# Kernel tuning notes

Hardware: AMD Instinct MI355X
Metric: run time of the kernel (lower is better)

Reference implementation:

```python
import jax, jax.numpy as jnp
import numpy as np

B, D, K, H, E, Z = 64, 25000, 16, 128, 256, 32


def setup_inputs() -> dict:
    key = jax.random.key(0)
    ks = jax.random.split(key, 10)
    s = 0.02
    return {
        "x": jax.random.normal(ks[0], (B, D), jnp.float32),
        "mask": jax.random.randint(ks[1], (B, D), 0, 2, jnp.int32),
        "feat_emb": jax.random.normal(ks[2], (D, K), jnp.float32),          # feature_embedding [D,K]
        "feat_bias": jnp.zeros((D, 1), jnp.float32),                        # feature_bias [D,1]
        "W1": jax.random.normal(ks[3], (1 + K + 1, H), jnp.float32) * s,    # h_layer linear 1 (in,out)
        "b1": jnp.zeros((H,), jnp.float32),
        "W2": jax.random.normal(ks[4], (H, K), jnp.float32) * s,            # h_layer linear 2
        "b2": jnp.zeros((K,), jnp.float32),
        "We1": jax.random.normal(ks[5], (K, E), jnp.float32) * s,           # encoder_mlp linear 1
        "be1": jnp.zeros((E,), jnp.float32),
        "We2": jax.random.normal(ks[6], (E, 2 * Z), jnp.float32) * s,       # encoder_mlp linear 2
        "be2": jnp.zeros((2 * Z,), jnp.float32),
    }


def reference(x, mask, feat_emb, feat_bias, W1, b1, W2, b2, We1, be1, We2, be2):
    b, d = x.shape
    k = feat_emb.shape[1]
    # Build per-(sample, feature) input rows: [x_bd, F_d(K), bias_d] -> [B, D, 1+K+1]
    h_in = jnp.concatenate(
        [
            x[:, :, None],
            jnp.broadcast_to(feat_emb[None, :, :], (b, d, k)),
            jnp.broadcast_to(feat_bias[None, :, :], (b, d, 1)),
        ],
        axis=-1,
    )
    # Shared small MLP (h_layer), dropout is identity at rate 0.0
    h = jax.nn.relu(h_in @ W1 + b1)          # [B, D, H]
    h = jax.nn.relu(h @ W2 + b2)             # [B, D, K]
    # Masked sum pooling over features
    c = jnp.sum(h * mask.astype(h.dtype)[:, :, None], axis=1)  # [B, K]
    # encoder_mlp
    enc = jax.nn.relu(c @ We1 + be1) @ We2 + be2                # [B, 2Z]
    mu, logvar = jnp.split(enc, 2, axis=-1)
    return mu, logvar
```

## Files before the change

kernel.cpp:

```cpp
#include <hip/hip_runtime.h>

#define B 64
#define D 25000
#define K 16
#define H 128
#define E 256
#define Z 32
#define DTILE 16
#define NT_TILES ((D + DTILE - 1) / DTILE)
#define NPB 512
#define XSTR 68
#define MSTR 68

typedef __attribute__((ext_vector_type(8))) _Float16 half8;
typedef __attribute__((ext_vector_type(2))) _Float16 hv2;
typedef __attribute__((ext_vector_type(4))) float f32x4;

__global__ __launch_bounds__(256, 2) void main_kernel(
    const float* __restrict__ x, const int* __restrict__ mask,
    const float* __restrict__ feat_emb, const float* __restrict__ feat_bias,
    const float* __restrict__ W1, const float* __restrict__ b1,
    const float* __restrict__ W2, const float* __restrict__ b2,
    float* __restrict__ part)
{
    __shared__ __align__(16) _Float16 sGh[2][DTILE * H];
    __shared__ __align__(16) _Float16 sXh[2][DTILE * XSTR];
    __shared__ __align__(16) float    sMf[2][DTILE * MSTR];

    const int t    = threadIdx.x;
    const int lane = t & 63;
    const int wv   = t >> 6;
    const int g    = lane >> 4;
    const int n    = lane & 15;

    half8 Bf[4];
    #pragma unroll
    for (int s = 0; s < 4; ++s) {
        union { half8 v; _Float16 e[8]; } u;
        #pragma unroll
        for (int j = 0; j < 8; ++j)
            u.e[j] = (_Float16)W2[(s * 32 + g * 8 + j) * K + n];
        Bf[s] = u.v;
    }
    hv2 w0h[4][4];
    #pragma unroll
    for (int s = 0; s < 4; ++s) {
        const float4* wp = (const float4*)&W1[s * 32 + g * 8];
        float4 a0 = wp[0], a1 = wp[1];
        w0h[s][0] = (hv2){(_Float16)a0.x, (_Float16)a0.y};
        w0h[s][1] = (hv2){(_Float16)a0.z, (_Float16)a0.w};
        w0h[s][2] = (hv2){(_Float16)a1.x, (_Float16)a1.y};
        w0h[s][3] = (hv2){(_Float16)a1.z, (_Float16)a1.w};
    }
    half8 bfG[2];
    #pragma unroll
    for (int cc = 0; cc < 2; ++cc) {
        const int h = (wv * 2 + cc) * 16 + n;
        union { half8 v; _Float16 e[8]; } u;
        #pragma unroll
        for (int j = 0; j < 8; ++j) {
            const int k = g * 8 + j;
            float v;
            if (k < 16)       v = W1[(1 + k) * H + h];
            else if (k == 16) v = W1[17 * H + h];
            else if (k == 17) v = b1[h];
            else              v = 0.f;
            u.e[j] = (_Float16)v;
        }
        bfG[cc] = u.v;
    }
    const float b2n = b2[n];
    const hv2 zeroh = {(_Float16)0.f, (_Float16)0.f};
    const int moff = wv * 16 + g * 4;
    const int sample = wv * 16 + n;

    auto STAGE = [&](int buf, int tile) {
        const int bb = t >> 2;
        const int dd = (t & 3) * 4;
        const int dg = tile * DTILE + dd;
        float xv[4], mv[4];
        if (dg + 4 <= D) {
            float4 xx = *(const float4*)&x[(size_t)bb * D + dg];
            int4   mm = *(const int4*)&mask[(size_t)bb * D + dg];
            xv[0] = xx.x; xv[1] = xx.y; xv[2] = xx.z; xv[3] = xx.w;
            mv[0] = (float)mm.x; mv[1] = (float)mm.y; mv[2] = (float)mm.z; mv[3] = (float)mm.w;
        } else {
            #pragma unroll
            for (int i = 0; i < 4; ++i) {
                const int dgi = dg + i;
                xv[i] = (dgi < D) ? x[(size_t)bb * D + dgi] : 0.f;
                mv[i] = (dgi < D) ? (float)mask[(size_t)bb * D + dgi] : 0.f;
            }
        }
        #pragma unroll
        for (int i = 0; i < 4; ++i) {
            sXh[buf][(dd + i) * XSTR + bb] = (_Float16)xv[i];
            sMf[buf][(dd + i) * MSTR + bb] = mv[i];
        }
    };

    auto GCOMP = [&](int buf, int tile) {
        const int dA = min(tile * DTILE + n, D - 1);
        union { half8 v; _Float16 e[8]; } af;
        if (g < 2) {
            const float4* fe = (const float4*)&feat_emb[(size_t)dA * K + g * 8];
            float4 u0 = fe[0], u1 = fe[1];
            af.e[0] = (_Float16)u0.x; af.e[1] = (_Float16)u0.y;
            af.e[2] = (_Float16)u0.z; af.e[3] = (_Float16)u0.w;
            af.e[4] = (_Float16)u1.x; af.e[5] = (_Float16)u1.y;
            af.e[6] = (_Float16)u1.z; af.e[7] = (_Float16)u1.w;
        } else if (g == 2) {
            af.e[0] = (_Float16)feat_bias[dA];
            af.e[1] = (_Float16)1.f;
            #pragma unroll
            for (int j = 2; j < 8; ++j) af.e[j] = (_Float16)0.f;
        } else {
            #pragma unroll
            for (int j = 0; j < 8; ++j) af.e[j] = (_Float16)0.f;
        }
        #pragma unroll
        for (int cc = 0; cc < 2; ++cc) {
            f32x4 C = {0.f, 0.f, 0.f, 0.f};
            C = __builtin_amdgcn_mfma_f32_16x16x32_f16(af.v, bfG[cc], C, 0, 0, 0);
            #pragma unroll
            for (int r = 0; r < 4; ++r)
                sGh[buf][(g * 4 + r) * H + (wv * 2 + cc) * 16 + n] = (_Float16)C[r];
        }
    };

    f32x4 cacc = {0.f, 0.f, 0.f, 0.f};

    int tt = blockIdx.x;
    STAGE(0, tt);
    GCOMP(0, tt);
    __syncthreads();

    int cur = 0;
    for (; tt < NT_TILES; tt += NPB) {
        const int nxt = tt + NPB;
        if (nxt < NT_TILES) { STAGE(cur ^ 1, nxt); GCOMP(cur ^ 1, nxt); }

        hv2 xh[DTILE / 2];
        #pragma unroll
        for (int i = 0; i < DTILE / 2; ++i)
            xh[i] = (hv2){sXh[cur][(2 * i) * XSTR + sample],
                          sXh[cur][(2 * i + 1) * XSTR + sample]};
        const _Float16* gb0 = sGh[cur] + g * 8;

        #pragma unroll
        for (int i = 0; i < DTILE / 2; ++i) {
            const int dd0 = 2 * i, dd1 = 2 * i + 1;
            const hv2 xa = {xh[i].x, xh[i].x};
            const hv2 xb = {xh[i].y, xh[i].y};
            f32x4 c1a = {b2n, b2n, b2n, b2n};
            f32x4 c1b = {b2n, b2n, b2n, b2n};
            #pragma unroll
            for (int s = 0; s < 4; ++s) {
                union GA { half8 v; hv2 p[4]; };
                GA ga, gb, A0, A1;
                ga.v = *(const half8*)(gb0 + dd0 * H + s * 32);
                gb.v = *(const half8*)(gb0 + dd1 * H + s * 32);
                #pragma unroll
                for (int p = 0; p < 4; ++p) {
                    hv2 h0 = __builtin_elementwise_fma(xa, w0h[s][p], ga.p[p]);
                    hv2 h1 = __builtin_elementwise_fma(xb, w0h[s][p], gb.p[p]);
                    A0.p[p] = __builtin_elementwise_max(h0, zeroh);
                    A1.p[p] = __builtin_elementwise_max(h1, zeroh);
                }
                c1a = __builtin_amdgcn_mfma_f32_16x16x32_f16(A0.v, Bf[s], c1a, 0, 0, 0);
                c1b = __builtin_amdgcn_mfma_f32_16x16x32_f16(A1.v, Bf[s], c1b, 0, 0, 0);
            }
            float4 m0 = *(const float4*)&sMf[cur][dd0 * MSTR + moff];
            float4 m1 = *(const float4*)&sMf[cur][dd1 * MSTR + moff];
            cacc[0] = fmaf(m0.x, fmaxf(c1a[0], 0.f), fmaf(m1.x, fmaxf(c1b[0], 0.f), cacc[0]));
            cacc[1] = fmaf(m0.y, fmaxf(c1a[1], 0.f), fmaf(m1.y, fmaxf(c1b[1], 0.f), cacc[1]));
            cacc[2] = fmaf(m0.z, fmaxf(c1a[2], 0.f), fmaf(m1.z, fmaxf(c1b[2], 0.f), cacc[2]));
            cacc[3] = fmaf(m0.w, fmaxf(c1a[3], 0.f), fmaf(m1.w, fmaxf(c1b[3], 0.f), cacc[3]));
        }
        __syncthreads();
        cur ^= 1;
    }

    float* crep = part + (size_t)blockIdx.x * (B * K);
    #pragma unroll
    for (int r = 0; r < 4; ++r)
        crep[(moff + r) * K + n] = cacc[r];
}

__global__ __launch_bounds__(256) void partial_enc_kernel(
    const float* __restrict__ part, const float* __restrict__ We1,
    const float* __restrict__ be1, const float* __restrict__ We2,
    const float* __restrict__ be2, float* __restrict__ out)
{
    const int b = blockIdx.x;
    const int t = threadIdx.x;
    __shared__ float sc[K];
    __shared__ float st1[E];
    __shared__ float red[256];

    {
        const int k = t & 15;
        float acc0 = 0.f;
        #pragma unroll 4
        for (int p = t >> 4; p < NPB; p += 16)
            acc0 += part[(size_t)p * (B * K) + b * K + k];
        red[t] = acc0;
    }
    __syncthreads();
    if (t < K) {
        float s2 = 0.f;
        #pragma unroll
        for (int q = 0; q < 16; ++q) s2 += red[q * 16 + t];
        sc[t] = s2;
    }
    __syncthreads();

    {
        float acc = be1[t];
        #pragma unroll
        for (int k = 0; k < K; ++k)
            acc = fmaf(sc[k], We1[k * E + t], acc);
        st1[t] = fmaxf(acc, 0.f);
    }
    __syncthreads();

    const int j = t & 63, seg = t >> 6;
    float acc = 0.f;
    #pragma unroll 4
    for (int e = seg * 64; e < seg * 64 + 64; ++e)
        acc = fmaf(st1[e], We2[e * 64 + j], acc);
    red[t] = acc;
    __syncthreads();

    if (t < 64) {
        float v = red[j] + red[64 + j] + red[128 + j] + red[192 + j] + be2[j];
        if (j < Z) out[b * Z + j] = v;
        else       out[B * Z + b * Z + (j - Z)] = v;
    }
}

extern "C" void kernel_launch(void* const* d_in, const int* in_sizes, int n_in,
                              void* d_out, int out_size, void* d_ws, size_t ws_size,
                              hipStream_t stream) {
    const float* x         = (const float*)d_in[0];
    const int*   mask      = (const int*)  d_in[1];
    const float* feat_emb  = (const float*)d_in[2];
    const float* feat_bias = (const float*)d_in[3];
    const float* W1        = (const float*)d_in[4];
    const float* b1        = (const float*)d_in[5];
    const float* W2        = (const float*)d_in[6];
    const float* b2        = (const float*)d_in[7];
    const float* We1       = (const float*)d_in[8];
    const float* be1       = (const float*)d_in[9];
    const float* We2       = (const float*)d_in[10];
    const float* be2       = (const float*)d_in[11];

    float* part = (float*)d_ws;

    main_kernel<<<NPB, 256, 0, stream>>>(
        x, mask, feat_emb, feat_bias, W1, b1, W2, b2, part);
    partial_enc_kernel<<<B, 256, 0, stream>>>(
        part, We1, be1, We2, be2, (float*)d_out);
}
```

Measured before the change: 112.1 us.

## Split tile features across waves instead of samples and reduce partials in LDS

Each wave now handles 4 of the 16 features in a tile for all 64 samples, instead of 16 samples across all features. This lets each wave load the per-feature G vectors once and reuse them across four sample groups, and x is stored sample-major so it can be read as packed half4. Because waves now hold partial sums for the same outputs, a cross-wave LDS reduction runs before the global write. The partial buffer is laid out sample-major so the second kernel reads it contiguously. The cost is more accumulator registers and extra LDS, which may affect occupancy at 2 blocks per CU.

```diff
diff --git a/kernel.cpp b/kernel.cpp
--- a/kernel.cpp
+++ b/kernel.cpp
@@ -9,10 +9,11 @@
 #define DTILE 16
 #define NT_TILES ((D + DTILE - 1) / DTILE)
 #define NPB 512
-#define XSTR 68
-#define MSTR 68
+#define XROW 20
+#define MROWF 68
 
 typedef __attribute__((ext_vector_type(8))) _Float16 half8;
+typedef __attribute__((ext_vector_type(4))) _Float16 hv4;
 typedef __attribute__((ext_vector_type(2))) _Float16 hv2;
 typedef __attribute__((ext_vector_type(4))) float f32x4;
 
@@ -24,8 +25,9 @@
     float* __restrict__ part)
 {
     __shared__ __align__(16) _Float16 sGh[2][DTILE * H];
-    __shared__ __align__(16) _Float16 sXh[2][DTILE * XSTR];
-    __shared__ __align__(16) float    sMf[2][DTILE * MSTR];
+    __shared__ __align__(16) _Float16 sXb[2][B * XROW];
+    __shared__ __align__(16) float    sMf[2][DTILE * MROWF];
+    __shared__ __align__(16) float    sRed[4][B * K];
 
     const int t    = threadIdx.x;
     const int lane = t & 63;
@@ -71,8 +73,7 @@
     }
     const float b2n = b2[n];
     const hv2 zeroh = {(_Float16)0.f, (_Float16)0.f};
-    const int moff = wv * 16 + g * 4;
-    const int sample = wv * 16 + n;
+    const int ddb = wv * 4;
 
     auto STAGE = [&](int buf, int tile) {
         const int bb = t >> 2;
@@ -92,11 +93,11 @@
                 mv[i] = (dgi < D) ? (float)mask[(size_t)bb * D + dgi] : 0.f;
             }
         }
-        #pragma unroll
-        for (int i = 0; i < 4; ++i) {
-            sXh[buf][(dd + i) * XSTR + bb] = (_Float16)xv[i];
-            sMf[buf][(dd + i) * MSTR + bb] = mv[i];
-        }
+        hv4 xp = {(_Float16)xv[0], (_Float16)xv[1], (_Float16)xv[2], (_Float16)xv[3]};
+        *(hv4*)&sXb[buf][bb * XROW + dd] = xp;
+        #pragma unroll
+        for (int i = 0; i < 4; ++i)
+            sMf[buf][(dd + i) * MROWF + bb] = mv[i];
     };
 
     auto GCOMP = [&](int buf, int tile) {
@@ -128,7 +129,7 @@
         }
     };
 
-    f32x4 cacc = {0.f, 0.f, 0.f, 0.f};
+    f32x4 cacc[4] = {{0.f,0.f,0.f,0.f},{0.f,0.f,0.f,0.f},{0.f,0.f,0.f,0.f},{0.f,0.f,0.f,0.f}};
 
     int tt = blockIdx.x;
     STAGE(0, tt);
@@ -140,51 +141,58 @@
         const int nxt = tt + NPB;
         if (nxt < NT_TILES) { STAGE(cur ^ 1, nxt); GCOMP(cur ^ 1, nxt); }
 
-        hv2 xh[DTILE / 2];
-        #pragma unroll
-        for (int i = 0; i < DTILE / 2; ++i)
-            xh[i] = (hv2){sXh[cur][(2 * i) * XSTR + sample],
-                          sXh[cur][(2 * i + 1) * XSTR + sample]};
-        const _Float16* gb0 = sGh[cur] + g * 8;
-
-        #pragma unroll
-        for (int i = 0; i < DTILE / 2; ++i) {
-            const int dd0 = 2 * i, dd1 = 2 * i + 1;
-            const hv2 xa = {xh[i].x, xh[i].x};
-            const hv2 xb = {xh[i].y, xh[i].y};
-            f32x4 c1a = {b2n, b2n, b2n, b2n};
-            f32x4 c1b = {b2n, b2n, b2n, b2n};
-            #pragma unroll
-            for (int s = 0; s < 4; ++s) {
-                union GA { half8 v; hv2 p[4]; };
-                GA ga, gb, A0, A1;
-                ga.v = *(const half8*)(gb0 + dd0 * H + s * 32);
-                gb.v = *(const half8*)(gb0 + dd1 * H + s * 32);
+        hv4 xq[4];
+        #pragma unroll
+        for (int m = 0; m < 4; ++m)
+            xq[m] = *(const hv4*)&sXb[cur][(m * 16 + n) * XROW + ddb];
+
+        #pragma unroll
+        for (int i = 0; i < 4; ++i) {
+            const int dd = ddb + i;
+            half8 Gv[4];
+            #pragma unroll
+            for (int s = 0; s < 4; ++s)
+                Gv[s] = *(const half8*)&sGh[cur][dd * H + s * 32 + g * 8];
+            #pragma unroll
+            for (int m = 0; m < 4; ++m) {
+                const _Float16 xs = xq[m][i];
+                const hv2 xx = {xs, xs};
+                f32x4 c1 = {b2n, b2n, b2n, b2n};
                 #pragma unroll
-                for (int p = 0; p < 4; ++p) {
-                    hv2 h0 = __builtin_elementwise_fma(xa, w0h[s][p], ga.p[p]);
-                    hv2 h1 = __builtin_elementwise_fma(xb, w0h[s][p], gb.p[p]);
-                    A0.p[p] = __builtin_elementwise_max(h0, zeroh);
-                    A1.p[p] = __builtin_elementwise_max(h1, zeroh);
+                for (int s = 0; s < 4; ++s) {
+                    union GA { half8 v; hv2 p[4]; };
+                    GA gg, A0;
+                    gg.v = Gv[s];
+                    #pragma unroll
+                    for (int p = 0; p < 4; ++p) {
+                        hv2 h0 = __builtin_elementwise_fma(xx, w0h[s][p], gg.p[p]);
+                        A0.p[p] = __builtin_elementwise_max(h0, zeroh);
+                    }
+                    c1 = __builtin_amdgcn_mfma_f32_16x16x32_f16(A0.v, Bf[s], c1, 0, 0, 0);
                 }
-                c1a = __builtin_amdgcn_mfma_f32_16x16x32_f16(A0.v, Bf[s], c1a, 0, 0, 0);
-                c1b = __builtin_amdgcn_mfma_f32_16x16x32_f16(A1.v, Bf[s], c1b, 0, 0, 0);
+                float4 mk = *(const float4*)&sMf[cur][dd * MROWF + m * 16 + g * 4];
+                cacc[m][0] = fmaf(mk.x, fmaxf(c1[0], 0.f), cacc[m][0]);
+                cacc[m][1] = fmaf(mk.y, fmaxf(c1[1], 0.f), cacc[m][1]);
+                cacc[m][2] = fmaf(mk.z, fmaxf(c1[2], 0.f), cacc[m][2]);
+                cacc[m][3] = fmaf(mk.w, fmaxf(c1[3], 0.f), cacc[m][3]);
             }
-            float4 m0 = *(const float4*)&sMf[cur][dd0 * MSTR + moff];
-            float4 m1 = *(const float4*)&sMf[cur][dd1 * MSTR + moff];
-            cacc[0] = fmaf(m0.x, fmaxf(c1a[0], 0.f), fmaf(m1.x, fmaxf(c1b[0], 0.f), cacc[0]));
-            cacc[1] = fmaf(m0.y, fmaxf(c1a[1], 0.f), fmaf(m1.y, fmaxf(c1b[1], 0.f), cacc[1]));
-            cacc[2] = fmaf(m0.z, fmaxf(c1a[2], 0.f), fmaf(m1.z, fmaxf(c1b[2], 0.f), cacc[2]));
-            cacc[3] = fmaf(m0.w, fmaxf(c1a[3], 0.f), fmaf(m1.w, fmaxf(c1b[3], 0.f), cacc[3]));
         }
         __syncthreads();
         cur ^= 1;
     }
 
-    float* crep = part + (size_t)blockIdx.x * (B * K);
-    #pragma unroll
-    for (int r = 0; r < 4; ++r)
-        crep[(moff + r) * K + n] = cacc[r];
+    #pragma unroll
+    for (int m = 0; m < 4; ++m)
+        #pragma unroll
+        for (int r = 0; r < 4; ++r)
+            sRed[wv][(m * 16 + g * 4 + r) * K + n] = cacc[m][r];
+    __syncthreads();
+    #pragma unroll
+    for (int q = 0; q < 4; ++q) {
+        const int o = t + q * 256;
+        const float v = sRed[0][o] + sRed[1][o] + sRed[2][o] + sRed[3][o];
+        part[(size_t)(o >> 4) * (NPB * K) + (size_t)blockIdx.x * K + (o & 15)] = v;
+    }
 }
 
 __global__ __launch_bounds__(256) void partial_enc_kernel(
@@ -199,11 +207,11 @@
     __shared__ float red[256];
 
     {
-        const int k = t & 15;
+        const float* pb = part + (size_t)b * (NPB * K);
         float acc0 = 0.f;
-        #pragma unroll 4
-        for (int p = t >> 4; p < NPB; p += 16)
-            acc0 += part[(size_t)p * (B * K) + b * K + k];
+        #pragma unroll 8
+        for (int i = 0; i < (NPB * K) / 256; ++i)
+            acc0 += pb[t + i * 256];
         red[t] = acc0;
     }
     __syncthreads();
```

New measurement: 108.4 us. 1.03x faster.
